# Kernel tuning notes

Hardware: AMD Instinct MI355X
Metric: run time of the kernel (lower is better)

The kernel has to match this reference:

```python
import jax, jax.numpy as jnp
import numpy as np

NUM_DST = 100_000   # blk.num_dst()
E = 1_000_000       # number of temporal edges
U_N = 200_000       # unique node rows
U_E = 100_000       # unique edge-feature rows
U_T = 100_000       # unique time deltas
DN, DE, DT, DOUT, H = 172, 172, 100, 100, 2
NEG_SLOPE = 0.2
LN_EPS = 1e-5


def _lin_init(k, fan_in, fan_out):
    return jax.random.normal(k, (fan_in, fan_out), jnp.float32) / np.float32(np.sqrt(fan_in))


def setup_inputs() -> dict:
    key = jax.random.key(0)
    ks = jax.random.split(key, 16)
    return {
        "nodeData": jax.random.normal(ks[0], (U_N, DN), jnp.float32),
        "efeat_unique": jax.random.normal(ks[1], (U_E, DE), jnp.float32),
        "unique_time_delta": jax.random.uniform(ks[2], (U_T,), jnp.float32) * 1000.0,
        "reverse_nids": jax.random.randint(ks[3], (NUM_DST + E,), 0, U_N, jnp.int32),
        "reverse_eids": jax.random.randint(ks[4], (E,), 0, U_E, jnp.int32),
        "reverse_time_delta": jax.random.randint(ks[5], (E,), 0, U_T, jnp.int32),
        "dstindex": jax.random.randint(ks[6], (E,), 0, NUM_DST, jnp.int32),
        "num_dst": NUM_DST,
        "time_w": jax.random.normal(ks[7], (DT,), jnp.float32),
        "time_b": jax.random.normal(ks[8], (DT,), jnp.float32),
        "Wqn": _lin_init(ks[9], DN, DOUT), "bqn": jnp.zeros((DOUT,), jnp.float32),
        "Wqt": _lin_init(ks[10], DT, DOUT), "bqt": jnp.zeros((DOUT,), jnp.float32),
        "Wkvn": _lin_init(ks[11], DN, 2 * DOUT), "bkvn": jnp.zeros((2 * DOUT,), jnp.float32),
        "Wkve": _lin_init(ks[12], DE, 2 * DOUT), "bkve": jnp.zeros((2 * DOUT,), jnp.float32),
        "Wkvt": _lin_init(ks[13], DT, 2 * DOUT), "bkvt": jnp.zeros((2 * DOUT,), jnp.float32),
        "Wout": _lin_init(ks[14], DN + DOUT, DOUT), "bout": jnp.zeros((DOUT,), jnp.float32),
        "ln_g": jnp.ones((DOUT,), jnp.float32), "ln_b": jnp.zeros((DOUT,), jnp.float32),
    }


def _forward(nodeData, efeat_unique, unique_time_delta, time_w, time_b,
             Wqn, bqn, Wqt, bqt, Wkvn, bkvn, Wkve, bkve, Wkvt, bkvt,
             Wout, bout, ln_g, ln_b,
             reverse_nids, reverse_eids, reverse_time_delta, dstindex, num_dst):
    node_dst_inv = reverse_nids[:num_dst]   # dst -> unique node row
    node_inv = reverse_nids[num_dst:]       # edge -> unique node row (src/nbr)
    # TimeEncode: cos(t * w + b); t=0 for all dst nodes (single shared row).
    nbrs_time_feat = jnp.cos(unique_time_delta[:, None] * time_w[None, :] + time_b[None, :])  # [U_T, DT]
    time_dst = jnp.cos(time_b)[None, :]                                                       # [1, DT]
    # Queries: project unique tables once, then gather (dedup trick).
    q = (nodeData @ Wqn + bqn)[node_dst_inv] + (time_dst @ Wqt + bqt)  # [num_dst, DOUT]
    Q = q[dstindex]                                                    # [E, DOUT]
    # Keys/values: fused node+edge+time projections, gathered per edge.
    Z = ((nodeData @ Wkvn + bkvn)[node_inv]
         + (efeat_unique @ Wkve + bkve)[reverse_eids]
         + (nbrs_time_feat @ Wkvt + bkvt)[reverse_time_delta])         # [E, 2*DOUT]
    dh = DOUT // H
    K = Z[:, :DOUT].reshape(-1, H, dh)
    V = Z[:, DOUT:].reshape(-1, H, dh)
    Qh = Q.reshape(-1, H, dh)
    attn = jax.nn.leaky_relu(jnp.sum(Qh * K, axis=2), NEG_SLOPE)       # [E, H]
    # edge softmax over incoming edges of each dst node
    m = jax.lax.stop_gradient(jax.ops.segment_max(attn, dstindex, num_segments=num_dst))
    e = jnp.exp(attn - m[dstindex])
    s = jax.ops.segment_sum(e, dstindex, num_segments=num_dst)
    a = e / s[dstindex]                                                # [E, H]
    # edge reduce (sum) -> [num_dst, DOUT]
    out = jax.ops.segment_sum((V * a[:, :, None]).reshape(-1, DOUT), dstindex, num_segments=num_dst)
    out = jnp.concatenate([out, nodeData[node_dst_inv]], axis=1)       # [num_dst, DOUT+DN]
    out = jax.nn.relu(out @ Wout + bout)
    mu = out.mean(axis=-1, keepdims=True)
    var = out.var(axis=-1, keepdims=True)
    return (out - mu) / jnp.sqrt(var + LN_EPS) * ln_g + ln_b


def reference(nodeData, efeat_unique, unique_time_delta, reverse_nids, reverse_eids,
              reverse_time_delta, dstindex, num_dst, time_w, time_b,
              Wqn, bqn, Wqt, bqt, Wkvn, bkvn, Wkve, bkve, Wkvt, bkvt,
              Wout, bout, ln_g, ln_b):
    return _forward(nodeData, efeat_unique, unique_time_delta, time_w, time_b,
                    Wqn, bqn, Wqt, bqt, Wkvn, bkvn, Wkve, bkve, Wkvt, bkvt,
                    Wout, bout, ln_g, ln_b,
                    reverse_nids, reverse_eids, reverse_time_delta, dstindex, num_dst)
```

## Files before the change

### kernel.cpp

```cpp
#include <hip/hip_runtime.h>
#include <hip/hip_bf16.h>

typedef __hip_bfloat16 bf16;

#define K_NUM_DST 100000
#define K_E       1000000
#define K_UN      200000
#define K_UE      100000
#define K_UT      100000
#define K_DN      172
#define K_DT      100
#define K_DOUT    100
#define K_DKV     200
#define K_DCAT    272
#define K_NEG_SLOPE 0.2f
#define K_LN_EPS    1e-5f

__device__ __forceinline__ float bits2f(unsigned short u){
  union { float f; unsigned int i; } c; c.i = ((unsigned int)u) << 16; return c.f;
}
__device__ __forceinline__ float t2f(float v){ return v; }
__device__ __forceinline__ float t2f(bf16 v){ return __bfloat162float(v); }

template<typename TIN> struct OutStore;
template<> struct OutStore<float>{
  static __device__ __forceinline__ void st(void* o, size_t i, float v){ ((float*)o)[i] = v; }
};
template<> struct OutStore<bf16>{
  static __device__ __forceinline__ void st(void* o, size_t i, float v){ ((bf16*)o)[i] = __float2bfloat16(v); }
};

template<typename TIN> struct Ld4;
template<> struct Ld4<float>{
  static __device__ __forceinline__ float4 ld(const void* base, size_t eo){
    return *(const float4*)((const float*)base + eo);
  }
};
template<> struct Ld4<bf16>{
  static __device__ __forceinline__ float4 ld(const void* base, size_t eo){
    ushort4 u = *(const ushort4*)((const unsigned short*)base + eo);
    float4 f; f.x = bits2f(u.x); f.y = bits2f(u.y); f.z = bits2f(u.z); f.w = bits2f(u.w);
    return f;
  }
};

template<typename TAB> __device__ __forceinline__ void store4(TAB* p, float a, float b, float c, float d);
template<> __device__ __forceinline__ void store4<float>(float* p, float a, float b, float c, float d){
  float4 v; v.x=a; v.y=b; v.z=c; v.w=d; *(float4*)p = v;
}
template<> __device__ __forceinline__ void store4<bf16>(bf16* p, float a, float b, float c, float d){
  p[0]=__float2bfloat16(a); p[1]=__float2bfloat16(b); p[2]=__float2bfloat16(c); p[3]=__float2bfloat16(d);
}

__global__ void detect_kernel(const unsigned short* __restrict__ nd, int* __restrict__ dflag){
  unsigned int i = blockIdx.x * 256u + threadIdx.x;
  unsigned short u = nd[i];
  if (((u >> 7) & 0xFF) == 0xFF) atomicOr(dflag, 1);
}

template<typename TIN>
__global__ void qt_kernel(const int* __restrict__ dflag, int want,
                          const void* time_b_v, const void* Wqt_v,
                          const void* bqt_v, float* __restrict__ qt){
  if (*dflag != want) return;
  const TIN* time_b = (const TIN*)time_b_v;
  const TIN* Wqt = (const TIN*)Wqt_v;
  const TIN* bqt = (const TIN*)bqt_v;
  int c = threadIdx.x;
  if (c >= K_DOUT) return;
  float acc = t2f(bqt[c]);
  for (int k = 0; k < K_DT; k++)
    acc += cosf(t2f(time_b[k])) * t2f(Wqt[k * K_DOUT + c]);
  qt[c] = acc;
}

template<typename TAB, typename TIN>
__global__ __launch_bounds__(320)
void node_proj_kernel(const int* __restrict__ dflag, int want,
    const void* nodeData_v, const void* Wqn_v, const void* bqn_v,
    const void* Wkvn_v, const void* bkvn_v,
    TAB* __restrict__ qn_tab, TAB* __restrict__ kvn_tab){
  if (*dflag != want) return;
  __shared__ float xs[32][180];
  int row0 = blockIdx.x * 32;
  int tid = threadIdx.x;
  for (int idx = tid; idx < 32 * 43; idx += 320){
    int r = idx / 43, kk = idx % 43;
    float4 v = Ld4<TIN>::ld(nodeData_v, (size_t)(row0 + r) * K_DN + kk * 4);
    *(float4*)&xs[r][kk * 4] = v;
  }
  __syncthreads();
  if (tid >= 300) return;
  int ci = tid % 75, ri = tid / 75;
  const void* W; const TIN* B; int ldw, c0;
  if (ci < 25){ W = Wqn_v;  B = (const TIN*)bqn_v;  ldw = K_DOUT; c0 = 4*ci; }
  else        { W = Wkvn_v; B = (const TIN*)bkvn_v; ldw = K_DKV;  c0 = 4*(ci-25); }
  float acc[8][4] = {};
  const float* xbase = &xs[8*ri][0];
  for (int kk = 0; kk < 43; kk++){
    int k = 4 * kk;
    float4 w0 = Ld4<TIN>::ld(W, (size_t)(k+0) * ldw + c0);
    float4 w1 = Ld4<TIN>::ld(W, (size_t)(k+1) * ldw + c0);
    float4 w2 = Ld4<TIN>::ld(W, (size_t)(k+2) * ldw + c0);
    float4 w3 = Ld4<TIN>::ld(W, (size_t)(k+3) * ldw + c0);
    #pragma unroll
    for (int i = 0; i < 8; i++){
      float4 a = *(const float4*)(xbase + i * 180 + k);
      acc[i][0] = fmaf(a.x,w0.x, fmaf(a.y,w1.x, fmaf(a.z,w2.x, fmaf(a.w,w3.x, acc[i][0]))));
      acc[i][1] = fmaf(a.x,w0.y, fmaf(a.y,w1.y, fmaf(a.z,w2.y, fmaf(a.w,w3.y, acc[i][1]))));
      acc[i][2] = fmaf(a.x,w0.z, fmaf(a.y,w1.z, fmaf(a.z,w2.z, fmaf(a.w,w3.z, acc[i][2]))));
      acc[i][3] = fmaf(a.x,w0.w, fmaf(a.y,w1.w, fmaf(a.z,w2.w, fmaf(a.w,w3.w, acc[i][3]))));
    }
  }
  float b0 = t2f(B[c0+0]), b1 = t2f(B[c0+1]), b2 = t2f(B[c0+2]), b3 = t2f(B[c0+3]);
  TAB* tab = (ci < 25) ? qn_tab : kvn_tab;
  #pragma unroll
  for (int i = 0; i < 8; i++){
    size_t row = row0 + 8*ri + i;
    store4<TAB>(&tab[row * ldw + c0], acc[i][0]+b0, acc[i][1]+b1, acc[i][2]+b2, acc[i][3]+b3);
  }
}

template<typename TAB, typename TIN>
__global__ __launch_bounds__(256)
void feat_proj_kernel(const int* __restrict__ dflag, int want,
    const void* A_v, const void* W_v, const void* bias_v,
    TAB* __restrict__ out_tab){
  if (*dflag != want) return;
  __shared__ float xs[40][180];
  int row0 = blockIdx.x * 40;
  int tid = threadIdx.x;
  for (int idx = tid; idx < 40 * 43; idx += 256){
    int r = idx / 43, kk = idx % 43;
    float4 v = Ld4<TIN>::ld(A_v, (size_t)(row0 + r) * K_DN + kk * 4);
    *(float4*)&xs[r][kk * 4] = v;
  }
  __syncthreads();
  if (tid >= 250) return;
  int ci = tid % 50, ri = tid / 50;
  int c0 = 4 * ci;
  float acc[8][4] = {};
  const float* xbase = &xs[8*ri][0];
  for (int kk = 0; kk < 43; kk++){
    int k = 4 * kk;
    float4 w0 = Ld4<TIN>::ld(W_v, (size_t)(k+0) * K_DKV + c0);
    float4 w1 = Ld4<TIN>::ld(W_v, (size_t)(k+1) * K_DKV + c0);
    float4 w2 = Ld4<TIN>::ld(W_v, (size_t)(k+2) * K_DKV + c0);
    float4 w3 = Ld4<TIN>::ld(W_v, (size_t)(k+3) * K_DKV + c0);
    #pragma unroll
    for (int i = 0; i < 8; i++){
      float4 a = *(const float4*)(xbase + i * 180 + k);
      acc[i][0] = fmaf(a.x,w0.x, fmaf(a.y,w1.x, fmaf(a.z,w2.x, fmaf(a.w,w3.x, acc[i][0]))));
      acc[i][1] = fmaf(a.x,w0.y, fmaf(a.y,w1.y, fmaf(a.z,w2.y, fmaf(a.w,w3.y, acc[i][1]))));
      acc[i][2] = fmaf(a.x,w0.z, fmaf(a.y,w1.z, fmaf(a.z,w2.z, fmaf(a.w,w3.z, acc[i][2]))));
      acc[i][3] = fmaf(a.x,w0.w, fmaf(a.y,w1.w, fmaf(a.z,w2.w, fmaf(a.w,w3.w, acc[i][3]))));
    }
  }
  const TIN* B = (const TIN*)bias_v;
  float b0 = t2f(B[c0+0]), b1 = t2f(B[c0+1]), b2 = t2f(B[c0+2]), b3 = t2f(B[c0+3]);
  #pragma unroll
  for (int i = 0; i < 8; i++){
    size_t row = row0 + 8*ri + i;
    store4<TAB>(&out_tab[row * K_DKV + c0], acc[i][0]+b0, acc[i][1]+b1, acc[i][2]+b2, acc[i][3]+b3);
  }
}

template<typename TAB, typename TIN>
__global__ __launch_bounds__(256)
void time_proj_kernel(const int* __restrict__ dflag, int want,
    const void* utd_v, const void* time_w_v, const void* time_b_v,
    const void* Wkvt_v, const void* bkvt_v,
    TAB* __restrict__ kvt_tab){
  if (*dflag != want) return;
  __shared__ float xs[40][104];
  __shared__ float ts[40];
  int row0 = blockIdx.x * 40;
  int tid = threadIdx.x;
  if (tid < 40) ts[tid] = t2f(((const TIN*)utd_v)[row0 + tid]);
  __syncthreads();
  for (int idx = tid; idx < 40 * K_DT; idx += 256){
    int r = idx / K_DT, k = idx % K_DT;
    xs[r][k] = cosf(ts[r] * t2f(((const TIN*)time_w_v)[k]) + t2f(((const TIN*)time_b_v)[k]));
  }
  __syncthreads();
  if (tid >= 250) return;
  int ci = tid % 50, ri = tid / 50;
  int c0 = 4 * ci;
  float acc[8][4] = {};
  const float* xbase = &xs[8*ri][0];
  for (int kk = 0; kk < 25; kk++){
    int k = 4 * kk;
    float4 w0 = Ld4<TIN>::ld(Wkvt_v, (size_t)(k+0) * K_DKV + c0);
    float4 w1 = Ld4<TIN>::ld(Wkvt_v, (size_t)(k+1) * K_DKV + c0);
    float4 w2 = Ld4<TIN>::ld(Wkvt_v, (size_t)(k+2) * K_DKV + c0);
    float4 w3 = Ld4<TIN>::ld(Wkvt_v, (size_t)(k+3) * K_DKV + c0);
    #pragma unroll
    for (int i = 0; i < 8; i++){
      float4 a = *(const float4*)(xbase + i * 104 + k);
      acc[i][0] = fmaf(a.x,w0.x, fmaf(a.y,w1.x, fmaf(a.z,w2.x, fmaf(a.w,w3.x, acc[i][0]))));
      acc[i][1] = fmaf(a.x,w0.y, fmaf(a.y,w1.y, fmaf(a.z,w2.y, fmaf(a.w,w3.y, acc[i][1]))));
      acc[i][2] = fmaf(a.x,w0.z, fmaf(a.y,w1.z, fmaf(a.z,w2.z, fmaf(a.w,w3.z, acc[i][2]))));
      acc[i][3] = fmaf(a.x,w0.w, fmaf(a.y,w1.w, fmaf(a.z,w2.w, fmaf(a.w,w3.w, acc[i][3]))));
    }
  }
  const TIN* B = (const TIN*)bkvt_v;
  float b0 = t2f(B[c0+0]), b1 = t2f(B[c0+1]), b2 = t2f(B[c0+2]), b3 = t2f(B[c0+3]);
  #pragma unroll
  for (int i = 0; i < 8; i++){
    size_t row = row0 + 8*ri + i;
    store4<TAB>(&kvt_tab[row * K_DKV + c0], acc[i][0]+b0, acc[i][1]+b1, acc[i][2]+b2, acc[i][3]+b3);
  }
}

__global__ void hist_kernel(const int* __restrict__ dstindex, int* __restrict__ counts){
  int e = blockIdx.x * blockDim.x + threadIdx.x;
  if (e < K_E) atomicAdd(&counts[dstindex[e]], 1);
}

__global__ void scan1_kernel(const int* __restrict__ counts, int* __restrict__ offsets,
                             int* __restrict__ bsum, int n){
  __shared__ int sd[256];
  int b = blockIdx.x, t = threadIdx.x;
  int base = b * 1024 + t * 4;
  int v0=0,v1=0,v2=0,v3=0;
  if (base+0 < n) v0 = counts[base+0];
  if (base+1 < n) v1 = counts[base+1];
  if (base+2 < n) v2 = counts[base+2];
  if (base+3 < n) v3 = counts[base+3];
  int s = v0+v1+v2+v3;
  sd[t] = s;
  __syncthreads();
  for (int off = 1; off < 256; off <<= 1){
    int tmp = (t >= off) ? sd[t-off] : 0;
    __syncthreads();
    sd[t] += tmp;
    __syncthreads();
  }
  int excl = sd[t] - s;
  if (base+0 < n) offsets[base+0] = excl;
  if (base+1 < n) offsets[base+1] = excl + v0;
  if (base+2 < n) offsets[base+2] = excl + v0 + v1;
  if (base+3 < n) offsets[base+3] = excl + v0 + v1 + v2;
  if (t == 255) bsum[b] = sd[255];
}

__global__ void scan2_kernel(int* bsum, int nb){
  if (threadIdx.x == 0 && blockIdx.x == 0){
    int run = 0;
    for (int i = 0; i < nb; i++){ int v = bsum[i]; bsum[i] = run; run += v; }
  }
}

__global__ void scan3_kernel(int* __restrict__ offsets, const int* __restrict__ bsum, int n){
  int i = blockIdx.x * blockDim.x + threadIdx.x;
  if (i < n) offsets[i] += bsum[i >> 10];
}

__global__ void scatter_kernel(const int* __restrict__ dstindex, const int* __restrict__ offsets,
                               int* __restrict__ cursor, int* __restrict__ edge_ids){
  int e = blockIdx.x * blockDim.x + threadIdx.x;
  if (e < K_E){
    int d = dstindex[e];
    int p = atomicAdd(&cursor[d], 1);
    edge_ids[offsets[d] + p] = e;
  }
}

template<typename TAB>
__global__ __launch_bounds__(256)
void attn_kernel(
    const int* __restrict__ reverse_nids, const int* __restrict__ reverse_eids,
    const int* __restrict__ reverse_tids,
    const int* __restrict__ dstoff, const int* __restrict__ dstcnt,
    const int* __restrict__ edge_ids,
    const TAB* __restrict__ qn_tab, const TAB* __restrict__ kvn_tab,
    const TAB* __restrict__ kve_tab, const TAB* __restrict__ kvt_tab,
    const float* __restrict__ qt, float* __restrict__ out_agg){
  int tid = threadIdx.x;
  int wave = tid >> 6;
  int l = tid & 63;
  int h = l >> 5;
  int li = l & 31;
  int dst = blockIdx.x * 4 + wave;
  int start = dstoff[dst];
  int cnt = dstcnt[dst];
  int cntw = (cnt + 1 - h) >> 1;
  bool act = (li < 25);
  int d4 = 4 * li;
  bool c0h0 = (d4+0) < 50, c1h0 = (d4+1) < 50, c2h0 = (d4+2) < 50, c3h0 = (d4+3) < 50;

  int gn = reverse_nids[dst];
  float4 q = make_float4(0.f,0.f,0.f,0.f);
  if (act){
    float4 qn = Ld4<TAB>::ld(qn_tab, (size_t)gn * K_DOUT + d4);
    float4 qtv = *(const float4*)(qt + d4);
    q.x = qn.x + qtv.x; q.y = qn.y + qtv.y; q.z = qn.z + qtv.z; q.w = qn.w + qtv.w;
  }

  float m0 = -3.0e38f, m1 = -3.0e38f, s0 = 0.f, s1 = 0.f;
  float ax = 0.f, ay = 0.f, az = 0.f, aw = 0.f;

  for (int j = 0; j < cntw; j++){
    int e   = edge_ids[start + 2*j + h];
    int nid = reverse_nids[K_NUM_DST + e];
    int eid = reverse_eids[e];
    int tde = reverse_tids[e];
    float4 kx = make_float4(0.f,0.f,0.f,0.f);
    if (act){
      float4 k1 = Ld4<TAB>::ld(kvn_tab, (size_t)nid * K_DKV + d4);
      float4 k2 = Ld4<TAB>::ld(kve_tab, (size_t)eid * K_DKV + d4);
      float4 k3 = Ld4<TAB>::ld(kvt_tab, (size_t)tde * K_DKV + d4);
      kx.x = k1.x+k2.x+k3.x; kx.y = k1.y+k2.y+k3.y; kx.z = k1.z+k2.z+k3.z; kx.w = k1.w+k2.w+k3.w;
    }
    float px = q.x*kx.x, py = q.y*kx.y, pz = q.z*kx.z, pw = q.w*kx.w;
    float p0 = (c0h0?px:0.f) + (c1h0?py:0.f) + (c2h0?pz:0.f) + (c3h0?pw:0.f);
    float p1 = (px+py+pz+pw) - p0;
    #pragma unroll
    for (int off = 16; off; off >>= 1){
      p0 += __shfl_xor(p0, off);
      p1 += __shfl_xor(p1, off);
    }
    float a0 = (p0 > 0.f) ? p0 : K_NEG_SLOPE * p0;
    float a1 = (p1 > 0.f) ? p1 : K_NEG_SLOPE * p1;
    float nm0 = fmaxf(m0, a0), nm1 = fmaxf(m1, a1);
    float al0 = __expf(m0 - nm0), al1 = __expf(m1 - nm1);
    float e0  = __expf(a0 - nm0), e1  = __expf(a1 - nm1);
    s0 = s0 * al0 + e0; s1 = s1 * al1 + e1;
    m0 = nm0; m1 = nm1;
    float4 vx = make_float4(0.f,0.f,0.f,0.f);
    if (act){
      float4 v1 = Ld4<TAB>::ld(kvn_tab, (size_t)nid * K_DKV + K_DOUT + d4);
      float4 v2 = Ld4<TAB>::ld(kve_tab, (size_t)eid * K_DKV + K_DOUT + d4);
      float4 v3 = Ld4<TAB>::ld(kvt_tab, (size_t)tde * K_DKV + K_DOUT + d4);
      vx.x = v1.x+v2.x+v3.x; vx.y = v1.y+v2.y+v3.y; vx.z = v1.z+v2.z+v3.z; vx.w = v1.w+v2.w+v3.w;
    }
    ax = ax * (c0h0?al0:al1) + (c0h0?e0:e1) * vx.x;
    ay = ay * (c1h0?al0:al1) + (c1h0?e0:e1) * vx.y;
    az = az * (c2h0?al0:al1) + (c2h0?e0:e1) * vx.z;
    aw = aw * (c3h0?al0:al1) + (c3h0?e0:e1) * vx.w;
  }

  float mo0 = __shfl_xor(m0, 32), so0 = __shfl_xor(s0, 32);
  float mo1 = __shfl_xor(m1, 32), so1 = __shfl_xor(s1, 32);
  float aox = __shfl_xor(ax, 32), aoy = __shfl_xor(ay, 32);
  float aoz = __shfl_xor(az, 32), aow = __shfl_xor(aw, 32);
  float M0 = fmaxf(m0, mo0), M1 = fmaxf(m1, mo1);
  float cs0 = __expf(m0 - M0), co0 = __expf(mo0 - M0);
  float cs1 = __expf(m1 - M1), co1 = __expf(mo1 - M1);
  float S0 = s0 * cs0 + so0 * co0;
  float S1 = s1 * cs1 + so1 * co1;
  float inv0 = (S0 > 0.f) ? 1.f / S0 : 0.f;
  float inv1 = (S1 > 0.f) ? 1.f / S1 : 0.f;
  float rx = c0h0 ? (ax*cs0 + aox*co0)*inv0 : (ax*cs1 + aox*co1)*inv1;
  float ry = c1h0 ? (ay*cs0 + aoy*co0)*inv0 : (ay*cs1 + aoy*co1)*inv1;
  float rz = c2h0 ? (az*cs0 + aoz*co0)*inv0 : (az*cs1 + aoz*co1)*inv1;
  float rw = c3h0 ? (aw*cs0 + aow*co0)*inv0 : (aw*cs1 + aow*co1)*inv1;
  if (h == 0 && act){
    float4 r; r.x=rx; r.y=ry; r.z=rz; r.w=rw;
    *(float4*)(out_agg + (size_t)dst * K_DOUT + d4) = r;
  }
}

template<typename TIN>
__global__ __launch_bounds__(256)
void final_kernel(const int* __restrict__ dflag, int want,
    const float* __restrict__ out_agg,
    const void* nodeData_v, const int* __restrict__ reverse_nids,
    const void* Wout_v, const void* bout_v,
    const void* ln_g_v, const void* ln_b_v,
    void* out){
  if (*dflag != want) return;
  __shared__ float xT[K_DCAT][36];
  __shared__ float y[32][104];
  __shared__ float stats[32][2];
  __shared__ int gnid[32];
  int dbase = blockIdx.x * 32;
  int tid = threadIdx.x;
  if (tid < 32) gnid[tid] = reverse_nids[dbase + tid];
  __syncthreads();
  for (int idx = tid; idx < 32 * 25; idx += 256){
    int r = idx / 25, kk = idx % 25;
    float4 v = *(const float4*)(out_agg + (size_t)(dbase + r) * K_DOUT + kk * 4);
    xT[kk*4+0][r] = v.x; xT[kk*4+1][r] = v.y; xT[kk*4+2][r] = v.z; xT[kk*4+3][r] = v.w;
  }
  for (int idx = tid; idx < 32 * 43; idx += 256){
    int r = idx / 43, kk = idx % 43;
    float4 v = Ld4<TIN>::ld(nodeData_v, (size_t)gnid[r] * K_DN + kk * 4);
    xT[K_DOUT + kk*4+0][r] = v.x; xT[K_DOUT + kk*4+1][r] = v.y;
    xT[K_DOUT + kk*4+2][r] = v.z; xT[K_DOUT + kk*4+3][r] = v.w;
  }
  __syncthreads();
  int ci = tid % 25, ri = tid / 25;
  float acc[4][4] = {};
  int c0 = 4 * ci;
  if (tid < 200){
    #pragma unroll 4
    for (int k = 0; k < K_DCAT; k++){
      float4 a = *(const float4*)&xT[k][4*ri];
      float4 w = Ld4<TIN>::ld(Wout_v, (size_t)k * K_DOUT + c0);
      acc[0][0]=fmaf(a.x,w.x,acc[0][0]); acc[0][1]=fmaf(a.x,w.y,acc[0][1]); acc[0][2]=fmaf(a.x,w.z,acc[0][2]); acc[0][3]=fmaf(a.x,w.w,acc[0][3]);
      acc[1][0]=fmaf(a.y,w.x,acc[1][0]); acc[1][1]=fmaf(a.y,w.y,acc[1][1]); acc[1][2]=fmaf(a.y,w.z,acc[1][2]); acc[1][3]=fmaf(a.y,w.w,acc[1][3]);
      acc[2][0]=fmaf(a.z,w.x,acc[2][0]); acc[2][1]=fmaf(a.z,w.y,acc[2][1]); acc[2][2]=fmaf(a.z,w.z,acc[2][2]); acc[2][3]=fmaf(a.z,w.w,acc[2][3]);
      acc[3][0]=fmaf(a.w,w.x,acc[3][0]); acc[3][1]=fmaf(a.w,w.y,acc[3][1]); acc[3][2]=fmaf(a.w,w.z,acc[3][2]); acc[3][3]=fmaf(a.w,w.w,acc[3][3]);
    }
    const TIN* B = (const TIN*)bout_v;
    float b0 = t2f(B[c0+0]), b1 = t2f(B[c0+1]), b2 = t2f(B[c0+2]), b3 = t2f(B[c0+3]);
    #pragma unroll
    for (int i = 0; i < 4; i++){
      acc[i][0] = fmaxf(acc[i][0]+b0, 0.f);
      acc[i][1] = fmaxf(acc[i][1]+b1, 0.f);
      acc[i][2] = fmaxf(acc[i][2]+b2, 0.f);
      acc[i][3] = fmaxf(acc[i][3]+b3, 0.f);
      float4 v; v.x=acc[i][0]; v.y=acc[i][1]; v.z=acc[i][2]; v.w=acc[i][3];
      *(float4*)&y[4*ri + i][c0] = v;
    }
  }
  __syncthreads();
  {
    int r = tid >> 3, qq = tid & 7;
    float s1 = 0.f, s2 = 0.f;
    for (int cc = qq; cc < K_DOUT; cc += 8){ float v = y[r][cc]; s1 += v; s2 += v * v; }
    #pragma unroll
    for (int off = 4; off; off >>= 1){ s1 += __shfl_xor(s1, off, 8); s2 += __shfl_xor(s2, off, 8); }
    if (qq == 0){ stats[r][0] = s1; stats[r][1] = s2; }
  }
  __syncthreads();
  if (tid < 200){
    const TIN* G = (const TIN*)ln_g_v; const TIN* Bb = (const TIN*)ln_b_v;
    float g0 = t2f(G[c0+0]), g1 = t2f(G[c0+1]), g2 = t2f(G[c0+2]), g3 = t2f(G[c0+3]);
    float lb0 = t2f(Bb[c0+0]), lb1 = t2f(Bb[c0+1]), lb2 = t2f(Bb[c0+2]), lb3 = t2f(Bb[c0+3]);
    #pragma unroll
    for (int i = 0; i < 4; i++){
      int r = 4*ri + i;
      float mu = stats[r][0] * (1.f / K_DOUT);
      float var = stats[r][1] * (1.f / K_DOUT) - mu * mu;
      float rs = rsqrtf(var + K_LN_EPS);
      size_t o = (size_t)(dbase + r) * K_DOUT + c0;
      OutStore<TIN>::st(out, o+0, (acc[i][0]-mu)*rs*g0 + lb0);
      OutStore<TIN>::st(out, o+1, (acc[i][1]-mu)*rs*g1 + lb1);
      OutStore<TIN>::st(out, o+2, (acc[i][2]-mu)*rs*g2 + lb2);
      OutStore<TIN>::st(out, o+3, (acc[i][3]-mu)*rs*g3 + lb3);
    }
  }
}

static inline size_t al256(size_t b){ return (b + 255) & ~(size_t)255; }

template<typename TAB>
static void run_pipeline(void* const* d_in, void* out, char* ws, hipStream_t stream){
  const void* nodeData = d_in[0];
  const void* efeat    = d_in[1];
  const void* utd      = d_in[2];
  const int* reverse_nids = (const int*)d_in[3];
  const int* reverse_eids = (const int*)d_in[4];
  const int* reverse_tids = (const int*)d_in[5];
  const int* dstindex     = (const int*)d_in[6];
  const void* time_w = d_in[8];
  const void* time_b = d_in[9];
  const void* Wqn  = d_in[10]; const void* bqn  = d_in[11];
  const void* Wqt  = d_in[12]; const void* bqt  = d_in[13];
  const void* Wkvn = d_in[14]; const void* bkvn = d_in[15];
  const void* Wkve = d_in[16]; const void* bkve = d_in[17];
  const void* Wkvt = d_in[18]; const void* bkvt = d_in[19];
  const void* Wout = d_in[20]; const void* bout = d_in[21];
  const void* ln_g = d_in[22]; const void* ln_b = d_in[23];

  char* p = ws;
  int* dflag = (int*)p;       p += 256;
  TAB* qn_tab  = (TAB*)p; p += al256(sizeof(TAB) * (size_t)K_UN * K_DOUT);
  TAB* kvn_tab = (TAB*)p; p += al256(sizeof(TAB) * (size_t)K_UN * K_DKV);
  TAB* kve_tab = (TAB*)p; p += al256(sizeof(TAB) * (size_t)K_UE * K_DKV);
  TAB* kvt_tab = (TAB*)p; p += al256(sizeof(TAB) * (size_t)K_UT * K_DKV);
  float* out_agg = (float*)p; p += al256(sizeof(float) * (size_t)K_NUM_DST * K_DOUT);
  float* qt = (float*)p;      p += al256(sizeof(float) * K_DOUT);
  int* counts = (int*)p;      p += al256(sizeof(int) * K_NUM_DST);
  int* offsets = (int*)p;     p += al256(sizeof(int) * K_NUM_DST);
  int* cursor = (int*)p;      p += al256(sizeof(int) * K_NUM_DST);
  int* bsum = (int*)p;        p += al256(sizeof(int) * 512);
  int* edge_ids = (int*)p;    p += al256(sizeof(int) * (size_t)K_E);

  hipMemsetAsync(dflag, 0, 256, stream);
  hipMemsetAsync(counts, 0, sizeof(int) * K_NUM_DST, stream);
  hipMemsetAsync(cursor, 0, sizeof(int) * K_NUM_DST, stream);

  detect_kernel<<<512, 256, 0, stream>>>((const unsigned short*)nodeData, dflag);

  qt_kernel<float><<<1, 128, 0, stream>>>(dflag, 1, time_b, Wqt, bqt, qt);
  node_proj_kernel<TAB, float><<<K_UN / 32, 320, 0, stream>>>(dflag, 1, nodeData, Wqn, bqn, Wkvn, bkvn, qn_tab, kvn_tab);
  feat_proj_kernel<TAB, float><<<K_UE / 40, 256, 0, stream>>>(dflag, 1, efeat, Wkve, bkve, kve_tab);
  time_proj_kernel<TAB, float><<<K_UT / 40, 256, 0, stream>>>(dflag, 1, utd, time_w, time_b, Wkvt, bkvt, kvt_tab);
  qt_kernel<bf16><<<1, 128, 0, stream>>>(dflag, 0, time_b, Wqt, bqt, qt);
  node_proj_kernel<TAB, bf16><<<K_UN / 32, 320, 0, stream>>>(dflag, 0, nodeData, Wqn, bqn, Wkvn, bkvn, qn_tab, kvn_tab);
  feat_proj_kernel<TAB, bf16><<<K_UE / 40, 256, 0, stream>>>(dflag, 0, efeat, Wkve, bkve, kve_tab);
  time_proj_kernel<TAB, bf16><<<K_UT / 40, 256, 0, stream>>>(dflag, 0, utd, time_w, time_b, Wkvt, bkvt, kvt_tab);

  hist_kernel<<<(K_E + 255) / 256, 256, 0, stream>>>(dstindex, counts);
  int nb = (K_NUM_DST + 1023) / 1024;
  scan1_kernel<<<nb, 256, 0, stream>>>(counts, offsets, bsum, K_NUM_DST);
  scan2_kernel<<<1, 1, 0, stream>>>(bsum, nb);
  scan3_kernel<<<(K_NUM_DST + 255) / 256, 256, 0, stream>>>(offsets, bsum, K_NUM_DST);
  scatter_kernel<<<(K_E + 255) / 256, 256, 0, stream>>>(dstindex, offsets, cursor, edge_ids);

  attn_kernel<TAB><<<K_NUM_DST / 4, 256, 0, stream>>>(reverse_nids, reverse_eids, reverse_tids,
      offsets, counts, edge_ids, qn_tab, kvn_tab, kve_tab, kvt_tab, qt, out_agg);

  final_kernel<float><<<K_NUM_DST / 32, 256, 0, stream>>>(dflag, 1, out_agg, nodeData, reverse_nids,
      Wout, bout, ln_g, ln_b, out);
  final_kernel<bf16><<<K_NUM_DST / 32, 256, 0, stream>>>(dflag, 0, out_agg, nodeData, reverse_nids,
      Wout, bout, ln_g, ln_b, out);
}

extern "C" void kernel_launch(void* const* d_in, const int* in_sizes, int n_in,
                              void* d_out, int out_size, void* d_ws, size_t ws_size,
                              hipStream_t stream){
  (void)in_sizes; (void)n_in; (void)out_size;

  size_t fixed = 256 + al256(4ull * K_NUM_DST * K_DOUT) + al256(4 * K_DOUT)
               + 3 * al256(4 * K_NUM_DST) + al256(4 * 512) + al256(4ull * K_E);
  size_t tab_elems = (size_t)K_UN * K_DOUT + (size_t)K_UN * K_DKV
                   + (size_t)K_UE * K_DKV + (size_t)K_UT * K_DKV;
  size_t need_f32  = fixed + tab_elems * 4 + 8192;
  size_t need_bf16 = fixed + tab_elems * 2 + 8192;

  if (ws_size >= need_f32){
    run_pipeline<float>(d_in, d_out, (char*)d_ws, stream);
  } else if (ws_size >= need_bf16){
    run_pipeline<bf16>(d_in, d_out, (char*)d_ws, stream);
  }
}
```

Baseline: 1.738 ms.

## Stream K-dimension in chunks to shrink shared memory in projection and final kernels

The projection kernels (node, feature, time) and the final output kernel now stage input rows into shared memory in K-chunks of 64 or 68 columns rather than the whole row. This cuts LDS per block and is meant to allow more resident blocks per CU. The final kernel also drops its transposed layout for a row-major chunk buffer with 4-wide K FMA groups. It computes LayerNorm statistics from per-thread partial sums instead of re-reading a full y tile. The cost is extra __syncthreads per chunk and less latency hiding inside each block.

```diff
diff --git a/kernel.cpp b/kernel.cpp
--- a/kernel.cpp
+++ b/kernel.cpp
@@ -81,37 +81,45 @@
     const void* Wkvn_v, const void* bkvn_v,
     TAB* __restrict__ qn_tab, TAB* __restrict__ kvn_tab){
   if (*dflag != want) return;
-  __shared__ float xs[32][180];
+  __shared__ float xs[32][64];
   int row0 = blockIdx.x * 32;
   int tid = threadIdx.x;
-  for (int idx = tid; idx < 32 * 43; idx += 320){
-    int r = idx / 43, kk = idx % 43;
-    float4 v = Ld4<TIN>::ld(nodeData_v, (size_t)(row0 + r) * K_DN + kk * 4);
-    *(float4*)&xs[r][kk * 4] = v;
-  }
-  __syncthreads();
-  if (tid >= 300) return;
   int ci = tid % 75, ri = tid / 75;
   const void* W; const TIN* B; int ldw, c0;
   if (ci < 25){ W = Wqn_v;  B = (const TIN*)bqn_v;  ldw = K_DOUT; c0 = 4*ci; }
   else        { W = Wkvn_v; B = (const TIN*)bkvn_v; ldw = K_DKV;  c0 = 4*(ci-25); }
   float acc[8][4] = {};
-  const float* xbase = &xs[8*ri][0];
-  for (int kk = 0; kk < 43; kk++){
-    int k = 4 * kk;
-    float4 w0 = Ld4<TIN>::ld(W, (size_t)(k+0) * ldw + c0);
-    float4 w1 = Ld4<TIN>::ld(W, (size_t)(k+1) * ldw + c0);
-    float4 w2 = Ld4<TIN>::ld(W, (size_t)(k+2) * ldw + c0);
-    float4 w3 = Ld4<TIN>::ld(W, (size_t)(k+3) * ldw + c0);
-    #pragma unroll
-    for (int i = 0; i < 8; i++){
-      float4 a = *(const float4*)(xbase + i * 180 + k);
-      acc[i][0] = fmaf(a.x,w0.x, fmaf(a.y,w1.x, fmaf(a.z,w2.x, fmaf(a.w,w3.x, acc[i][0]))));
-      acc[i][1] = fmaf(a.x,w0.y, fmaf(a.y,w1.y, fmaf(a.z,w2.y, fmaf(a.w,w3.y, acc[i][1]))));
-      acc[i][2] = fmaf(a.x,w0.z, fmaf(a.y,w1.z, fmaf(a.z,w2.z, fmaf(a.w,w3.z, acc[i][2]))));
-      acc[i][3] = fmaf(a.x,w0.w, fmaf(a.y,w1.w, fmaf(a.z,w2.w, fmaf(a.w,w3.w, acc[i][3]))));
-    }
-  }
+  #pragma unroll
+  for (int c = 0; c < 3; c++){
+    const int ng = (c < 2) ? 16 : 11;
+    if (c > 0) __syncthreads();
+    for (int idx = tid; idx < 32 * ng; idx += 320){
+      int r = idx / ng, g = idx % ng;
+      float4 v = Ld4<TIN>::ld(nodeData_v, (size_t)(row0 + r) * K_DN + (16*c + g) * 4);
+      *(float4*)&xs[r][g * 4] = v;
+    }
+    __syncthreads();
+    if (tid < 300){
+      const float* xbase = &xs[8*ri][0];
+      #pragma unroll 2
+      for (int g = 0; g < ng; g++){
+        int kg = (16*c + g) * 4;
+        float4 w0 = Ld4<TIN>::ld(W, (size_t)(kg+0) * ldw + c0);
+        float4 w1 = Ld4<TIN>::ld(W, (size_t)(kg+1) * ldw + c0);
+        float4 w2 = Ld4<TIN>::ld(W, (size_t)(kg+2) * ldw + c0);
+        float4 w3 = Ld4<TIN>::ld(W, (size_t)(kg+3) * ldw + c0);
+        #pragma unroll
+        for (int i = 0; i < 8; i++){
+          float4 a = *(const float4*)(xbase + i * 64 + 4*g);
+          acc[i][0] = fmaf(a.x,w0.x, fmaf(a.y,w1.x, fmaf(a.z,w2.x, fmaf(a.w,w3.x, acc[i][0]))));
+          acc[i][1] = fmaf(a.x,w0.y, fmaf(a.y,w1.y, fmaf(a.z,w2.y, fmaf(a.w,w3.y, acc[i][1]))));
+          acc[i][2] = fmaf(a.x,w0.z, fmaf(a.y,w1.z, fmaf(a.z,w2.z, fmaf(a.w,w3.z, acc[i][2]))));
+          acc[i][3] = fmaf(a.x,w0.w, fmaf(a.y,w1.w, fmaf(a.z,w2.w, fmaf(a.w,w3.w, acc[i][3]))));
+        }
+      }
+    }
+  }
+  if (tid >= 300) return;
   float b0 = t2f(B[c0+0]), b1 = t2f(B[c0+1]), b2 = t2f(B[c0+2]), b3 = t2f(B[c0+3]);
   TAB* tab = (ci < 25) ? qn_tab : kvn_tab;
   #pragma unroll
@@ -127,35 +135,43 @@
     const void* A_v, const void* W_v, const void* bias_v,
     TAB* __restrict__ out_tab){
   if (*dflag != want) return;
-  __shared__ float xs[40][180];
+  __shared__ float xs[40][64];
   int row0 = blockIdx.x * 40;
   int tid = threadIdx.x;
-  for (int idx = tid; idx < 40 * 43; idx += 256){
-    int r = idx / 43, kk = idx % 43;
-    float4 v = Ld4<TIN>::ld(A_v, (size_t)(row0 + r) * K_DN + kk * 4);
-    *(float4*)&xs[r][kk * 4] = v;
-  }
-  __syncthreads();
-  if (tid >= 250) return;
   int ci = tid % 50, ri = tid / 50;
   int c0 = 4 * ci;
   float acc[8][4] = {};
-  const float* xbase = &xs[8*ri][0];
-  for (int kk = 0; kk < 43; kk++){
-    int k = 4 * kk;
-    float4 w0 = Ld4<TIN>::ld(W_v, (size_t)(k+0) * K_DKV + c0);
-    float4 w1 = Ld4<TIN>::ld(W_v, (size_t)(k+1) * K_DKV + c0);
-    float4 w2 = Ld4<TIN>::ld(W_v, (size_t)(k+2) * K_DKV + c0);
-    float4 w3 = Ld4<TIN>::ld(W_v, (size_t)(k+3) * K_DKV + c0);
-    #pragma unroll
-    for (int i = 0; i < 8; i++){
-      float4 a = *(const float4*)(xbase + i * 180 + k);
-      acc[i][0] = fmaf(a.x,w0.x, fmaf(a.y,w1.x, fmaf(a.z,w2.x, fmaf(a.w,w3.x, acc[i][0]))));
-      acc[i][1] = fmaf(a.x,w0.y, fmaf(a.y,w1.y, fmaf(a.z,w2.y, fmaf(a.w,w3.y, acc[i][1]))));
-      acc[i][2] = fmaf(a.x,w0.z, fmaf(a.y,w1.z, fmaf(a.z,w2.z, fmaf(a.w,w3.z, acc[i][2]))));
-      acc[i][3] = fmaf(a.x,w0.w, fmaf(a.y,w1.w, fmaf(a.z,w2.w, fmaf(a.w,w3.w, acc[i][3]))));
-    }
-  }
+  #pragma unroll
+  for (int c = 0; c < 3; c++){
+    const int ng = (c < 2) ? 16 : 11;
+    if (c > 0) __syncthreads();
+    for (int idx = tid; idx < 40 * ng; idx += 256){
+      int r = idx / ng, g = idx % ng;
+      float4 v = Ld4<TIN>::ld(A_v, (size_t)(row0 + r) * K_DN + (16*c + g) * 4);
+      *(float4*)&xs[r][g * 4] = v;
+    }
+    __syncthreads();
+    if (tid < 250){
+      const float* xbase = &xs[8*ri][0];
+      #pragma unroll 2
+      for (int g = 0; g < ng; g++){
+        int kg = (16*c + g) * 4;
+        float4 w0 = Ld4<TIN>::ld(W_v, (size_t)(kg+0) * K_DKV + c0);
+        float4 w1 = Ld4<TIN>::ld(W_v, (size_t)(kg+1) * K_DKV + c0);
+        float4 w2 = Ld4<TIN>::ld(W_v, (size_t)(kg+2) * K_DKV + c0);
+        float4 w3 = Ld4<TIN>::ld(W_v, (size_t)(kg+3) * K_DKV + c0);
+        #pragma unroll
+        for (int i = 0; i < 8; i++){
+          float4 a = *(const float4*)(xbase + i * 64 + 4*g);
+          acc[i][0] = fmaf(a.x,w0.x, fmaf(a.y,w1.x, fmaf(a.z,w2.x, fmaf(a.w,w3.x, acc[i][0]))));
+          acc[i][1] = fmaf(a.x,w0.y, fmaf(a.y,w1.y, fmaf(a.z,w2.y, fmaf(a.w,w3.y, acc[i][1]))));
+          acc[i][2] = fmaf(a.x,w0.z, fmaf(a.y,w1.z, fmaf(a.z,w2.z, fmaf(a.w,w3.z, acc[i][2]))));
+          acc[i][3] = fmaf(a.x,w0.w, fmaf(a.y,w1.w, fmaf(a.z,w2.w, fmaf(a.w,w3.w, acc[i][3]))));
+        }
+      }
+    }
+  }
+  if (tid >= 250) return;
   const TIN* B = (const TIN*)bias_v;
   float b0 = t2f(B[c0+0]), b1 = t2f(B[c0+1]), b2 = t2f(B[c0+2]), b3 = t2f(B[c0+3]);
   #pragma unroll
@@ -172,37 +188,47 @@
     const void* Wkvt_v, const void* bkvt_v,
     TAB* __restrict__ kvt_tab){
   if (*dflag != want) return;
-  __shared__ float xs[40][104];
+  __shared__ float xs[40][64];
   __shared__ float ts[40];
   int row0 = blockIdx.x * 40;
   int tid = threadIdx.x;
   if (tid < 40) ts[tid] = t2f(((const TIN*)utd_v)[row0 + tid]);
   __syncthreads();
-  for (int idx = tid; idx < 40 * K_DT; idx += 256){
-    int r = idx / K_DT, k = idx % K_DT;
-    xs[r][k] = cosf(ts[r] * t2f(((const TIN*)time_w_v)[k]) + t2f(((const TIN*)time_b_v)[k]));
-  }
-  __syncthreads();
-  if (tid >= 250) return;
   int ci = tid % 50, ri = tid / 50;
   int c0 = 4 * ci;
   float acc[8][4] = {};
-  const float* xbase = &xs[8*ri][0];
-  for (int kk = 0; kk < 25; kk++){
-    int k = 4 * kk;
-    float4 w0 = Ld4<TIN>::ld(Wkvt_v, (size_t)(k+0) * K_DKV + c0);
-    float4 w1 = Ld4<TIN>::ld(Wkvt_v, (size_t)(k+1) * K_DKV + c0);
-    float4 w2 = Ld4<TIN>::ld(Wkvt_v, (size_t)(k+2) * K_DKV + c0);
-    float4 w3 = Ld4<TIN>::ld(Wkvt_v, (size_t)(k+3) * K_DKV + c0);
-    #pragma unroll
-    for (int i = 0; i < 8; i++){
-      float4 a = *(const float4*)(xbase + i * 104 + k);
-      acc[i][0] = fmaf(a.x,w0.x, fmaf(a.y,w1.x, fmaf(a.z,w2.x, fmaf(a.w,w3.x, acc[i][0]))));
-      acc[i][1] = fmaf(a.x,w0.y, fmaf(a.y,w1.y, fmaf(a.z,w2.y, fmaf(a.w,w3.y, acc[i][1]))));
-      acc[i][2] = fmaf(a.x,w0.z, fmaf(a.y,w1.z, fmaf(a.z,w2.z, fmaf(a.w,w3.z, acc[i][2]))));
-      acc[i][3] = fmaf(a.x,w0.w, fmaf(a.y,w1.w, fmaf(a.z,w2.w, fmaf(a.w,w3.w, acc[i][3]))));
-    }
-  }
+  #pragma unroll
+  for (int c = 0; c < 2; c++){
+    const int ng = (c < 1) ? 16 : 9;
+    const int nk = ng * 4;
+    if (c > 0) __syncthreads();
+    for (int idx = tid; idx < 40 * nk; idx += 256){
+      int r = idx / nk, kloc = idx % nk;
+      int k = 64*c + kloc;
+      xs[r][kloc] = cosf(ts[r] * t2f(((const TIN*)time_w_v)[k]) + t2f(((const TIN*)time_b_v)[k]));
+    }
+    __syncthreads();
+    if (tid < 250){
+      const float* xbase = &xs[8*ri][0];
+      #pragma unroll 2
+      for (int g = 0; g < ng; g++){
+        int kg = 64*c + 4*g;
+        float4 w0 = Ld4<TIN>::ld(Wkvt_v, (size_t)(kg+0) * K_DKV + c0);
+        float4 w1 = Ld4<TIN>::ld(Wkvt_v, (size_t)(kg+1) * K_DKV + c0);
+        float4 w2 = Ld4<TIN>::ld(Wkvt_v, (size_t)(kg+2) * K_DKV + c0);
+        float4 w3 = Ld4<TIN>::ld(Wkvt_v, (size_t)(kg+3) * K_DKV + c0);
+        #pragma unroll
+        for (int i = 0; i < 8; i++){
+          float4 a = *(const float4*)(xbase + i * 64 + 4*g);
+          acc[i][0] = fmaf(a.x,w0.x, fmaf(a.y,w1.x, fmaf(a.z,w2.x, fmaf(a.w,w3.x, acc[i][0]))));
+          acc[i][1] = fmaf(a.x,w0.y, fmaf(a.y,w1.y, fmaf(a.z,w2.y, fmaf(a.w,w3.y, acc[i][1]))));
+          acc[i][2] = fmaf(a.x,w0.z, fmaf(a.y,w1.z, fmaf(a.z,w2.z, fmaf(a.w,w3.z, acc[i][2]))));
+          acc[i][3] = fmaf(a.x,w0.w, fmaf(a.y,w1.w, fmaf(a.z,w2.w, fmaf(a.w,w3.w, acc[i][3]))));
+        }
+      }
+    }
+  }
+  if (tid >= 250) return;
   const TIN* B = (const TIN*)bkvt_v;
   float b0 = t2f(B[c0+0]), b1 = t2f(B[c0+1]), b2 = t2f(B[c0+2]), b3 = t2f(B[c0+3]);
   #pragma unroll
@@ -370,39 +396,50 @@
     const void* ln_g_v, const void* ln_b_v,
     void* out){
   if (*dflag != want) return;
-  __shared__ float xT[K_DCAT][36];
-  __shared__ float y[32][104];
+  __shared__ float xs[32][72];
+  __shared__ float part[32][25][2];
   __shared__ float stats[32][2];
   __shared__ int gnid[32];
   int dbase = blockIdx.x * 32;
   int tid = threadIdx.x;
   if (tid < 32) gnid[tid] = reverse_nids[dbase + tid];
   __syncthreads();
-  for (int idx = tid; idx < 32 * 25; idx += 256){
-    int r = idx / 25, kk = idx % 25;
-    float4 v = *(const float4*)(out_agg + (size_t)(dbase + r) * K_DOUT + kk * 4);
-    xT[kk*4+0][r] = v.x; xT[kk*4+1][r] = v.y; xT[kk*4+2][r] = v.z; xT[kk*4+3][r] = v.w;
-  }
-  for (int idx = tid; idx < 32 * 43; idx += 256){
-    int r = idx / 43, kk = idx % 43;
-    float4 v = Ld4<TIN>::ld(nodeData_v, (size_t)gnid[r] * K_DN + kk * 4);
-    xT[K_DOUT + kk*4+0][r] = v.x; xT[K_DOUT + kk*4+1][r] = v.y;
-    xT[K_DOUT + kk*4+2][r] = v.z; xT[K_DOUT + kk*4+3][r] = v.w;
-  }
-  __syncthreads();
   int ci = tid % 25, ri = tid / 25;
+  int c0 = 4 * ci;
   float acc[4][4] = {};
-  int c0 = 4 * ci;
+  #pragma unroll
+  for (int c = 0; c < 4; c++){
+    if (c > 0) __syncthreads();
+    for (int idx = tid; idx < 32 * 17; idx += 256){
+      int r = idx / 17, g = idx % 17;
+      int gk = (c * 17 + g) * 4;
+      float4 v;
+      if (gk < 100) v = *(const float4*)(out_agg + (size_t)(dbase + r) * K_DOUT + gk);
+      else          v = Ld4<TIN>::ld(nodeData_v, (size_t)gnid[r] * K_DN + (gk - 100));
+      *(float4*)&xs[r][g * 4] = v;
+    }
+    __syncthreads();
+    if (tid < 200){
+      const float* xbase = &xs[4 * ri][0];
+      #pragma unroll 2
+      for (int g = 0; g < 17; g++){
+        int kg = (c * 17 + g) * 4;
+        float4 w0 = Ld4<TIN>::ld(Wout_v, (size_t)(kg+0) * K_DOUT + c0);
+        float4 w1 = Ld4<TIN>::ld(Wout_v, (size_t)(kg+1) * K_DOUT + c0);
+        float4 w2 = Ld4<TIN>::ld(Wout_v, (size_t)(kg+2) * K_DOUT + c0);
+        float4 w3 = Ld4<TIN>::ld(Wout_v, (size_t)(kg+3) * K_DOUT + c0);
+        #pragma unroll
+        for (int i = 0; i < 4; i++){
+          float4 a = *(const float4*)(xbase + i * 72 + 4*g);
+          acc[i][0] = fmaf(a.x,w0.x, fmaf(a.y,w1.x, fmaf(a.z,w2.x, fmaf(a.w,w3.x, acc[i][0]))));
+          acc[i][1] = fmaf(a.x,w0.y, fmaf(a.y,w1.y, fmaf(a.z,w2.y, fmaf(a.w,w3.y, acc[i][1]))));
+          acc[i][2] = fmaf(a.x,w0.z, fmaf(a.y,w1.z, fmaf(a.z,w2.z, fmaf(a.w,w3.z, acc[i][2]))));
+          acc[i][3] = fmaf(a.x,w0.w, fmaf(a.y,w1.w, fmaf(a.z,w2.w, fmaf(a.w,w3.w, acc[i][3]))));
+        }
+      }
+    }
+  }
   if (tid < 200){
-    #pragma unroll 4
-    for (int k = 0; k < K_DCAT; k++){
-      float4 a = *(const float4*)&xT[k][4*ri];
-      float4 w = Ld4<TIN>::ld(Wout_v, (size_t)k * K_DOUT + c0);
-      acc[0][0]=fmaf(a.x,w.x,acc[0][0]); acc[0][1]=fmaf(a.x,w.y,acc[0][1]); acc[0][2]=fmaf(a.x,w.z,acc[0][2]); acc[0][3]=fmaf(a.x,w.w,acc[0][3]);
-      acc[1][0]=fmaf(a.y,w.x,acc[1][0]); acc[1][1]=fmaf(a.y,w.y,acc[1][1]); acc[1][2]=fmaf(a.y,w.z,acc[1][2]); acc[1][3]=fmaf(a.y,w.w,acc[1][3]);
-      acc[2][0]=fmaf(a.z,w.x,acc[2][0]); acc[2][1]=fmaf(a.z,w.y,acc[2][1]); acc[2][2]=fmaf(a.z,w.z,acc[2][2]); acc[2][3]=fmaf(a.z,w.w,acc[2][3]);
-      acc[3][0]=fmaf(a.w,w.x,acc[3][0]); acc[3][1]=fmaf(a.w,w.y,acc[3][1]); acc[3][2]=fmaf(a.w,w.z,acc[3][2]); acc[3][3]=fmaf(a.w,w.w,acc[3][3]);
-    }
     const TIN* B = (const TIN*)bout_v;
     float b0 = t2f(B[c0+0]), b1 = t2f(B[c0+1]), b2 = t2f(B[c0+2]), b3 = t2f(B[c0+3]);
     #pragma unroll
@@ -411,18 +448,17 @@
       acc[i][1] = fmaxf(acc[i][1]+b1, 0.f);
       acc[i][2] = fmaxf(acc[i][2]+b2, 0.f);
       acc[i][3] = fmaxf(acc[i][3]+b3, 0.f);
-      float4 v; v.x=acc[i][0]; v.y=acc[i][1]; v.z=acc[i][2]; v.w=acc[i][3];
-      *(float4*)&y[4*ri + i][c0] = v;
+      float s1 = acc[i][0]+acc[i][1]+acc[i][2]+acc[i][3];
+      float s2 = acc[i][0]*acc[i][0]+acc[i][1]*acc[i][1]+acc[i][2]*acc[i][2]+acc[i][3]*acc[i][3];
+      part[4*ri + i][ci][0] = s1;
+      part[4*ri + i][ci][1] = s2;
     }
   }
   __syncthreads();
-  {
-    int r = tid >> 3, qq = tid & 7;
+  if (tid < 32){
     float s1 = 0.f, s2 = 0.f;
-    for (int cc = qq; cc < K_DOUT; cc += 8){ float v = y[r][cc]; s1 += v; s2 += v * v; }
-    #pragma unroll
-    for (int off = 4; off; off >>= 1){ s1 += __shfl_xor(s1, off, 8); s2 += __shfl_xor(s2, off, 8); }
-    if (qq == 0){ stats[r][0] = s1; stats[r][1] = s2; }
+    for (int j = 0; j < 25; j++){ s1 += part[tid][j][0]; s2 += part[tid][j][1]; }
+    stats[tid][0] = s1; stats[tid][1] = s2;
   }
   __syncthreads();
   if (tid < 200){
```

Measured after the change: 1.758 ms. Within noise of the previous version (+1.1%).
